# Kernel tuning notes

Measured on AMD Instinct MI355X. Metric: run time of the kernel, lower is better.

## Reference

```python
import jax, jax.numpy as jnp
import numpy as np


def setup_inputs() -> dict:
    key = jax.random.key(0)
    k1, k2, k3, k4 = jax.random.split(key, 4)
    batch, T, state_dim, action_dim = 64, 1024, 512, 128
    x0 = jax.random.normal(k1, (batch, state_dim), dtype=jnp.float32)
    us = jax.random.normal(k2, (batch, T, action_dim), dtype=jnp.float32)
    # Scale A so the 1024-step linear recurrence stays bounded (spectral radius < 1)
    A = jax.random.normal(k3, (state_dim, state_dim), dtype=jnp.float32) * (0.9 / np.sqrt(state_dim))
    B = jax.random.normal(k4, (action_dim, state_dim), dtype=jnp.float32) * (1.0 / np.sqrt(action_dim))
    return {"x0": x0, "us": us, "A": A, "B": B}


def reference(x0, us, A, B):
    """Linear SSM rollout: x_{t+1} = x_t @ A + u_t @ B, returns xs [batch, T, state_dim]."""
    us_t = jnp.swapaxes(us, 0, 1)  # [T, batch, action_dim]

    def step(x, u):
        x_next = x @ A + u @ B  # [batch, state_dim]
        return x_next, x_next

    _, xs = jax.lax.scan(step, x0, us_t)  # xs: [T, batch, state_dim]
    return jnp.swapaxes(xs, 0, 1)  # [batch, T, state_dim]
```

## Files before the change

kernel.cpp:

```cpp
#include <hip/hip_runtime.h>


typedef __attribute__((ext_vector_type(8))) short bf16x8;
typedef __attribute__((ext_vector_type(8))) unsigned short ushort8;
typedef __attribute__((ext_vector_type(4))) float f32x4;
typedef unsigned short ushort_t;

#define MFMA16(a, b, c) __builtin_amdgcn_mfma_f32_16x16x32_bf16(a, b, c, 0, 0, 0)

#define OFF_AT  0UL
#define OFF_AU  8912896UL
#define OFF_BT  15204352UL
#define OFF_BU  15335424UL
#define OFF_WT  15466496UL
#define OFF_Z   16515072UL
#define OFF_E1S 41680896UL
#define OFF_E2S 50069504UL

__host__ __device__ __forceinline__ int slot_of(int p) {
    if (p == 0) return 16;
    if (p <= 8) return p - 1;
    return 7 + (p >> 3);
}

__device__ __forceinline__ unsigned short f2bf(float f) {
    union { float f; unsigned u; } v; v.f = f;
    unsigned r = v.u + 0x7FFFu + ((v.u >> 16) & 1u);
    return (unsigned short)(r >> 16);
}

__device__ __forceinline__ int sel4(int4 v, int p) {
    return p == 0 ? v.x : p == 1 ? v.y : p == 2 ? v.z : v.w;
}

typedef __attribute__((address_space(3))) unsigned int as3_u32;
typedef __attribute__((address_space(1))) const unsigned int as1_u32;
__device__ __forceinline__ void gll16(const void* g, void* l) {
    __builtin_amdgcn_global_load_lds((as1_u32*)g, (as3_u32*)l, 16, 0, 0);
}

__global__ __launch_bounds__(256) void prep_kernel(const float* __restrict__ x0,
                                                   const float* __restrict__ A,
                                                   const float* __restrict__ B,
                                                   char* __restrict__ ws) {
    ushort_t* At1 = (ushort_t*)(ws + OFF_AT);
    ushort_t* Au1 = (ushort_t*)(ws + OFF_AU);
    ushort_t* Bt  = (ushort_t*)(ws + OFF_BT);
    ushort_t* Bu  = (ushort_t*)(ws + OFF_BU);
    ushort_t* X0b = (ushort_t*)(ws + OFF_E2S);
    long idx = (long)blockIdx.x * 256 + threadIdx.x;
    if (idx < 262144) {
        Au1[idx] = f2bf(A[idx]);
    } else if (idx < 524288) {
        long gi = idx - 262144;
        int n = (int)(gi >> 9), k = (int)(gi & 511);
        At1[gi] = f2bf(A[(long)k * 512 + n]);
    } else if (idx < 589824) {
        long i2 = idx - 524288;
        int kp = (int)(i2 >> 9), n = (int)(i2 & 511);
        ushort_t v = f2bf(B[i2]);
        Bt[(long)n * 128 + kp] = v;
        Bu[i2] = v;
    } else if (idx < 593920) {
        long gi = idx - 589824;
        long e0 = gi * 8;
        float4 v0 = *(const float4*)(x0 + e0);
        float4 v1 = *(const float4*)(x0 + e0 + 4);
        ushort8 h = { f2bf(v0.x), f2bf(v0.y), f2bf(v0.z), f2bf(v0.w),
                      f2bf(v1.x), f2bf(v1.y), f2bf(v1.z), f2bf(v1.w) };
        *(ushort8*)(X0b + e0) = h;
    } else {
        long gi2 = idx - 593920;
        if (gi2 < 262144) {
            int n = (int)(gi2 >> 9), k2 = (int)(gi2 & 511);
            At1[(long)16 * 262144 + gi2] = (n == k2) ? (ushort_t)0x3F80 : (ushort_t)0;
        }
    }
}

__device__ __forceinline__ void pow_tile(char* __restrict__ ws, ushort_t* ldsX,
                                         int d, int m_, int i_, int prod,
                                         int mb, int nb) {
    ushort_t* At = (ushort_t*)(ws + OFF_AT);
    ushort_t* Au = (ushort_t*)(ws + OFF_AU);
    const ushort_t *Xp, *Yp; ushort_t* outp;
    if (prod == 0) { Xp = At + (long)slot_of(m_) * 262144; Yp = Au + (long)slot_of(i_) * 262144; outp = At + (long)slot_of(d) * 262144; }
    else           { Xp = Au + (long)slot_of(i_) * 262144; Yp = At + (long)slot_of(m_) * 262144; outp = Au + (long)slot_of(d) * 262144; }

    int tid = threadIdx.x, w = tid >> 6, lane = tid & 63, q = lane >> 4, r = lane & 15;

    for (int i2 = tid; i2 < 64 * 64; i2 += 256) {
        int row = i2 >> 6, c8 = i2 & 63;
        ushort8 v = *(const ushort8*)(Xp + (long)(mb * 64 + row) * 512 + c8 * 8);
        *(ushort8*)&ldsX[row * 512 + ((c8 ^ (row & 7)) << 3)] = v;
    }
    __syncthreads();

    f32x4 acc[4][2];
    for (int a1 = 0; a1 < 4; a1++) for (int b1 = 0; b1 < 2; b1++) acc[a1][b1] = (f32x4){0.f, 0.f, 0.f, 0.f};

    int n0 = nb * 128 + w * 32;
    for (int kt = 0; kt < 16; kt++) {
        bf16x8 b0 = *(const bf16x8*)(Yp + (long)(n0 + r) * 512 + kt * 32 + q * 8);
        bf16x8 b1 = *(const bf16x8*)(Yp + (long)(n0 + 16 + r) * 512 + kt * 32 + q * 8);
        int g2 = kt * 4 + q;
#pragma unroll
        for (int mi = 0; mi < 4; mi++) {
            int row = mi * 16 + r;
            bf16x8 a = *(bf16x8*)&ldsX[row * 512 + ((g2 ^ (row & 7)) << 3)];
            acc[mi][0] = MFMA16(a, b0, acc[mi][0]);
            acc[mi][1] = MFMA16(a, b1, acc[mi][1]);
        }
    }
    for (int mi = 0; mi < 4; mi++) for (int nj = 0; nj < 2; nj++) {
        int m = mb * 64 + mi * 16 + q * 4, n = n0 + nj * 16 + r;
        for (int v = 0; v < 4; v++) outp[(long)(m + v) * 512 + n] = f2bf(acc[mi][nj][v]);
    }
}

__device__ __forceinline__ void wk_tile(char* __restrict__ ws, ushort_t* ldsX,
                                        int k8, int mb) {
    ushort_t* At = (ushort_t*)(ws + OFF_AT);
    ushort_t* Bu = (ushort_t*)(ws + OFF_BU);
    ushort_t* Bt = (ushort_t*)(ws + OFF_BT);
    ushort_t* Wt = (ushort_t*)(ws + OFF_WT);

    int tid = threadIdx.x, w = tid >> 6, lane = tid & 63, q = lane >> 4, r = lane & 15;

    if (k8 == 7) {
        for (int i2 = tid; i2 < 64 * 32; i2 += 256) {
            int row = i2 >> 5, c4 = i2 & 31;
            ushort4 v = *(const ushort4*)(Bt + (long)(mb * 64 + row) * 128 + c4 * 4);
            *(ushort4*)(Wt + (long)(mb * 64 + row) * 128 + c4 * 4) = v;
        }
        return;
    }

    int p = 7 - k8;
    const ushort_t* Xp = At + (long)slot_of(p) * 262144;
    for (int i2 = tid; i2 < 64 * 64; i2 += 256) {
        int row = i2 >> 6, c8 = i2 & 63;
        ushort8 v = *(const ushort8*)(Xp + (long)(mb * 64 + row) * 512 + c8 * 8);
        *(ushort8*)&ldsX[row * 512 + ((c8 ^ (row & 7)) << 3)] = v;
    }
    __syncthreads();

    f32x4 acc[4][2];
    for (int a1 = 0; a1 < 4; a1++) for (int b1 = 0; b1 < 2; b1++) acc[a1][b1] = (f32x4){0.f, 0.f, 0.f, 0.f};

    int n0 = w * 32;
    for (int kt = 0; kt < 16; kt++) {
        bf16x8 b0 = *(const bf16x8*)(Bu + (long)(n0 + r) * 512 + kt * 32 + q * 8);
        bf16x8 b1 = *(const bf16x8*)(Bu + (long)(n0 + 16 + r) * 512 + kt * 32 + q * 8);
        int g2 = kt * 4 + q;
#pragma unroll
        for (int mi = 0; mi < 4; mi++) {
            int row = mi * 16 + r;
            bf16x8 a = *(bf16x8*)&ldsX[row * 512 + ((g2 ^ (row & 7)) << 3)];
            acc[mi][0] = MFMA16(a, b0, acc[mi][0]);
            acc[mi][1] = MFMA16(a, b1, acc[mi][1]);
        }
    }
    ushort_t* Wp = Wt + (long)p * 65536;
    for (int mi = 0; mi < 4; mi++) for (int nj = 0; nj < 2; nj++) {
        int m = mb * 64 + mi * 16 + q * 4, n = n0 + nj * 16 + r;
        for (int v = 0; v < 4; v++) Wp[(long)(m + v) * 128 + n] = f2bf(acc[mi][nj][v]);
    }
}

__global__ __launch_bounds__(256) void pow_stage(char* __restrict__ ws,
                                                 const float* __restrict__ us,
                                                 int4 dd, int4 mm, int4 ii,
                                                 int dual, int wkbase,
                                                 int ubase, int ustart, int uend) {
    __shared__ ushort_t ldsX[64 * 512];
    int bx = blockIdx.x;

    if (ubase > 0 && bx >= ubase) {
        ushort_t* Z = (ushort_t*)(ws + OFF_Z);
        int tid = threadIdx.x;
        int nthr = (256 - ubase) * 256;
        for (long gi = ustart + (long)(bx - ubase) * 256 + tid; gi < uend; gi += nthr) {
            int row = (int)(gi >> 7), g8 = (int)(gi & 127);
            int c = row >> 6, b = row & 63;
            const float* src = us + (long)b * 131072 + c * 1024 + g8 * 8;
            float4 v0 = *(const float4*)src;
            float4 v1 = *(const float4*)(src + 4);
            ushort8 h = { f2bf(v0.x), f2bf(v0.y), f2bf(v0.z), f2bf(v0.w),
                          f2bf(v1.x), f2bf(v1.y), f2bf(v1.z), f2bf(v1.w) };
            *(ushort8*)(Z + (long)row * 1536 + 512 + g8 * 8) = h;
        }
        return;
    }
    if (wkbase > 0 && bx >= wkbase) {
        int widx = bx - wkbase;
        wk_tile(ws, ldsX, widx >> 3, widx & 7);
        return;
    }

    int nb = bx & 3, mb = (bx >> 2) & 7;
    int prod, pair;
    if (dual) { prod = (bx >> 5) & 1; pair = bx >> 6; }
    else      { prod = 0;             pair = bx >> 5; }
    int d = sel4(dd, pair), m_ = sel4(mm, pair), i_ = sel4(ii, pair);
    pow_tile(ws, ldsX, d, m_, i_, prod, mb, nb);
}

__global__ __launch_bounds__(256, 4) void e1g(char* __restrict__ ws) {
    __shared__ ushort_t Alds[64 * 64];
    __shared__ ushort_t Blds[128 * 64];
    const ushort_t* Z  = (const ushort_t*)(ws + OFF_Z);
    const ushort_t* Wt = (const ushort_t*)(ws + OFF_WT);
    ushort_t* E1s = (ushort_t*)(ws + OFF_E1S);

    int bx = blockIdx.x;
    int c = bx >> 2, nt = bx & 3;
    int tid = threadIdx.x, w = tid >> 6, lane = tid & 63, q = lane >> 4, r = lane & 15;
    int wr = w >> 1, wc = w & 1;
    int l8 = lane >> 3, srcg = (lane & 7) ^ l8;

    const ushort_t* Xb = Z + (long)c * 64 * 1536 + 512;

    f32x4 acc[2][4];
#pragma unroll
    for (int a1 = 0; a1 < 2; a1++)
#pragma unroll
        for (int b1 = 0; b1 < 4; b1++) acc[a1][b1] = (f32x4){0.f, 0.f, 0.f, 0.f};

    for (int s = 0; s < 16; s++) {
        int k0 = s * 64;
#pragma unroll
        for (int i = 0; i < 2; i++) {
            int row = i * 32 + w * 8 + l8;
            gll16(Xb + (long)row * 1536 + k0 + srcg * 8, &Alds[i * 2048 + w * 512]);
        }
        const ushort_t* Yb = Wt + (long)(7 - (s >> 1)) * 65536 + (s & 1) * 64;
#pragma unroll
        for (int i = 0; i < 4; i++) {
            int row = i * 32 + w * 8 + l8;
            gll16(Yb + (long)(nt * 128 + row) * 128 + srcg * 8, &Blds[i * 2048 + w * 512]);
        }
        __syncthreads();
#pragma unroll
        for (int kt = 0; kt < 2; kt++) {
            int g2 = kt * 4 + q;
            bf16x8 a[2], b[4];
#pragma unroll
            for (int mi = 0; mi < 2; mi++) {
                int row = wr * 32 + mi * 16 + r;
                a[mi] = *(bf16x8*)&Alds[row * 64 + ((g2 ^ (row & 7)) << 3)];
            }
#pragma unroll
            for (int nj = 0; nj < 4; nj++) {
                int row = wc * 64 + nj * 16 + r;
                b[nj] = *(bf16x8*)&Blds[row * 64 + ((g2 ^ (row & 7)) << 3)];
            }
#pragma unroll
            for (int mi = 0; mi < 2; mi++)
#pragma unroll
                for (int nj = 0; nj < 4; nj++)
                    acc[mi][nj] = MFMA16(a[mi], b[nj], acc[mi][nj]);
        }
        __syncthreads();
    }

#pragma unroll
    for (int mi = 0; mi < 2; mi++)
#pragma unroll
        for (int nj = 0; nj < 4; nj++) {
            int m = wr * 32 + mi * 16 + q * 4;
            int n = nt * 128 + wc * 64 + nj * 16 + r;
#pragma unroll
            for (int v = 0; v < 4; v++)
                E1s[(long)c * 32768 + (long)(m + v) * 512 + n] = f2bf(acc[mi][nj][v]);
        }
}

__global__ __launch_bounds__(256, 4) void e2g(char* __restrict__ ws) {
    __shared__ ushort_t Alds[64 * 64];
    __shared__ ushort_t Blds[32 * 64];
    const ushort_t* At  = (const ushort_t*)(ws + OFF_AT);
    const ushort_t* E1s = (const ushort_t*)(ws + OFF_E1S);
    ushort_t* E2s = (ushort_t*)(ws + OFF_E2S);

    int bx = blockIdx.x;
    int g = bx >> 4, ntb = bx & 15;
    int tid = threadIdx.x, w = tid >> 6, lane = tid & 63, q = lane >> 4, r = lane & 15;
    int wr = w >> 1, wc = w & 1;
    int l8 = lane >> 3, srcg = (lane & 7) ^ l8;

    f32x4 acc[2][1];
#pragma unroll
    for (int a1 = 0; a1 < 2; a1++) acc[a1][0] = (f32x4){0.f, 0.f, 0.f, 0.f};

    for (int s = 0; s < 64; s++) {
        int t = s >> 3, k0 = (s & 7) * 64;
        const ushort_t* Xp = E1s + (long)(8 * g + t) * 32768;
        const ushort_t* Yb = At + (long)slot_of(8 * (7 - t)) * 262144;
#pragma unroll
        for (int i = 0; i < 2; i++) {
            int row = i * 32 + w * 8 + l8;
            gll16(Xp + (long)row * 512 + k0 + srcg * 8, &Alds[i * 2048 + w * 512]);
        }
        {
            int row = w * 8 + l8;
            gll16(Yb + (long)(ntb * 32 + row) * 512 + k0 + srcg * 8, &Blds[w * 512]);
        }
        __syncthreads();
#pragma unroll
        for (int kt = 0; kt < 2; kt++) {
            int g2 = kt * 4 + q;
            bf16x8 a[2], b;
#pragma unroll
            for (int mi = 0; mi < 2; mi++) {
                int row = wr * 32 + mi * 16 + r;
                a[mi] = *(bf16x8*)&Alds[row * 64 + ((g2 ^ (row & 7)) << 3)];
            }
            {
                int row = wc * 16 + r;
                b = *(bf16x8*)&Blds[row * 64 + ((g2 ^ (row & 7)) << 3)];
            }
#pragma unroll
            for (int mi = 0; mi < 2; mi++)
                acc[mi][0] = MFMA16(a[mi], b, acc[mi][0]);
        }
        __syncthreads();
    }

#pragma unroll
    for (int mi = 0; mi < 2; mi++) {
        int m = wr * 32 + mi * 16 + q * 4;
        int n = ntb * 32 + wc * 16 + r;
#pragma unroll
        for (int v = 0; v < 4; v++)
            E2s[(long)(1 + g) * 32768 + (long)(m + v) * 512 + n] = f2bf(acc[mi][0][v]);
    }
}

__global__ __launch_bounds__(256, 4) void s1x(float* __restrict__ dout,
                                              char* __restrict__ ws) {
    __shared__ ushort_t Alds[64 * 64];
    __shared__ ushort_t Blds[128 * 64];
    const ushort_t* At  = (const ushort_t*)(ws + OFF_AT);
    const ushort_t* E1s = (const ushort_t*)(ws + OFF_E1S);
    const ushort_t* E2s = (const ushort_t*)(ws + OFF_E2S);
    ushort_t* Z = (ushort_t*)(ws + OFF_Z);

    int bx = blockIdx.x;
    int t0 = bx >> 2, nt = bx & 3;
    int g, j;
    if (t0 == 128) { g = 16; j = 0; }
    else {
        g = t0 >> 3;
        int jj = t0 & 7;
        j = (g >= 8) ? (7 - jj) : jj;
    }
    int c = g * 8 + j;
    int extra = (j == 0 && g >= 1) ? 1 : 0;
    int nterms = 1 + extra + j;
    int S = nterms * 8;
    int tid = threadIdx.x, w = tid >> 6, lane = tid & 63, q = lane >> 4, r = lane & 15;
    int wr = w >> 1, wc = w & 1;
    int l8 = lane >> 3, srcg = (lane & 7) ^ l8;

    auto xptr = [&](int t) -> const ushort_t* {
        if (t == 0) return E2s + (long)g * 32768;
        if (extra && t == 1) return E2s + (long)(g - 1) * 32768;
        return E1s + (long)(8 * g + t - 1 - extra) * 32768;
    };
    auto yptr = [&](int t) -> const ushort_t* {
        int p = (t == 0) ? 8 * j : ((extra && t == 1) ? 64 : 8 * (j - t + extra));
        return At + (long)slot_of(p) * 262144;
    };

    f32x4 acc[2][4];
#pragma unroll
    for (int a1 = 0; a1 < 2; a1++)
#pragma unroll
        for (int b1 = 0; b1 < 4; b1++) acc[a1][b1] = (f32x4){0.f, 0.f, 0.f, 0.f};

    for (int s = 0; s < S; s++) {
        int t = s >> 3, k0 = (s & 7) * 64;
        const ushort_t* Xp = xptr(t);
        const ushort_t* Yb = yptr(t);
#pragma unroll
        for (int i = 0; i < 2; i++) {
            int row = i * 32 + w * 8 + l8;
            gll16(Xp + (long)row * 512 + k0 + srcg * 8, &Alds[i * 2048 + w * 512]);
        }
#pragma unroll
        for (int i = 0; i < 4; i++) {
            int row = i * 32 + w * 8 + l8;
            gll16(Yb + (long)(nt * 128 + row) * 512 + k0 + srcg * 8, &Blds[i * 2048 + w * 512]);
        }
        __syncthreads();
#pragma unroll
        for (int kt = 0; kt < 2; kt++) {
            int g2 = kt * 4 + q;
            bf16x8 a[2], b[4];
#pragma unroll
            for (int mi = 0; mi < 2; mi++) {
                int row = wr * 32 + mi * 16 + r;
                a[mi] = *(bf16x8*)&Alds[row * 64 + ((g2 ^ (row & 7)) << 3)];
            }
#pragma unroll
            for (int nj = 0; nj < 4; nj++) {
                int row = wc * 64 + nj * 16 + r;
                b[nj] = *(bf16x8*)&Blds[row * 64 + ((g2 ^ (row & 7)) << 3)];
            }
#pragma unroll
            for (int mi = 0; mi < 2; mi++)
#pragma unroll
                for (int nj = 0; nj < 4; nj++)
                    acc[mi][nj] = MFMA16(a[mi], b[nj], acc[mi][nj]);
        }
        __syncthreads();
    }

#pragma unroll
    for (int mi = 0; mi < 2; mi++)
#pragma unroll
        for (int nj = 0; nj < 4; nj++) {
            int m = wr * 32 + mi * 16 + q * 4;
            int n = nt * 128 + wc * 64 + nj * 16 + r;
#pragma unroll
            for (int v = 0; v < 4; v++) {
                float val = acc[mi][nj][v];
                int row = m + v;
                if (c < 128)
                    Z[(long)(c * 64 + row) * 1536 + n] = f2bf(val);
                if (c >= 1)
                    dout[(long)row * 524288 + (long)(8 * c - 1) * 512 + n] = val;
            }
        }
}

__global__ __launch_bounds__(256, 4) void outg(float* __restrict__ dout,
                                               char* __restrict__ ws) {
    __shared__ ushort_t Alds[128 * 64];
    __shared__ ushort_t Blds[128 * 64];
    const ushort_t* Z  = (const ushort_t*)(ws + OFF_Z);
    const ushort_t* At = (const ushort_t*)(ws + OFF_AT);
    const ushort_t* Wt = (const ushort_t*)(ws + OFF_WT);

    int bx = blockIdx.x;
    int nt = bx / 448;
    int rem = bx - nt * 448;
    int k = rem >> 6;
    int mt = rem & 63;
    int tid = threadIdx.x, w = tid >> 6, lane = tid & 63, q = lane >> 4, r = lane & 15;
    int wr = w >> 1, wc = w & 1;
    int l8 = lane >> 3, srcg = (lane & 7) ^ l8;

    const ushort_t* Xb = Z + (long)mt * 128 * 1536;
    const ushort_t* Ya = At + (long)slot_of(k + 1) * 262144;
    int Ks = 8 + 2 * (k + 1);

    f32x4 acc[4][4];
#pragma unroll
    for (int a1 = 0; a1 < 4; a1++)
#pragma unroll
        for (int b1 = 0; b1 < 4; b1++) acc[a1][b1] = (f32x4){0.f, 0.f, 0.f, 0.f};

    for (int s = 0; s < Ks; s++) {
        int k0 = s * 64;
#pragma unroll
        for (int i = 0; i < 4; i++) {
            int row = i * 32 + w * 8 + l8;
            gll16(Xb + (long)row * 1536 + k0 + srcg * 8, &Alds[i * 2048 + w * 512]);
        }
        if (k0 < 512) {
#pragma unroll
            for (int i = 0; i < 4; i++) {
                int row = i * 32 + w * 8 + l8;
                gll16(Ya + (long)(nt * 128 + row) * 512 + k0 + srcg * 8, &Blds[i * 2048 + w * 512]);
            }
        } else {
            int uc = k0 - 512;
            const ushort_t* Yb = Wt + (long)(k - (uc >> 7)) * 65536 + (uc & 127);
#pragma unroll
            for (int i = 0; i < 4; i++) {
                int row = i * 32 + w * 8 + l8;
                gll16(Yb + (long)(nt * 128 + row) * 128 + srcg * 8, &Blds[i * 2048 + w * 512]);
            }
        }
        __syncthreads();
#pragma unroll
        for (int kt = 0; kt < 2; kt++) {
            int g2 = kt * 4 + q;
            bf16x8 a[4], b[4];
#pragma unroll
            for (int mi = 0; mi < 4; mi++) {
                int row = wr * 64 + mi * 16 + r;
                a[mi] = *(bf16x8*)&Alds[row * 64 + ((g2 ^ (row & 7)) << 3)];
            }
#pragma unroll
            for (int nj = 0; nj < 4; nj++) {
                int row = wc * 64 + nj * 16 + r;
                b[nj] = *(bf16x8*)&Blds[row * 64 + ((g2 ^ (row & 7)) << 3)];
            }
#pragma unroll
            for (int mi = 0; mi < 4; mi++)
#pragma unroll
                for (int nj = 0; nj < 4; nj++)
                    acc[mi][nj] = MFMA16(a[mi], b[nj], acc[mi][nj]);
        }
        __syncthreads();
    }

#pragma unroll
    for (int mi = 0; mi < 4; mi++) {
        int m = mt * 128 + wr * 64 + mi * 16 + q * 4;
#pragma unroll
        for (int nj = 0; nj < 4; nj++) {
            int n = nt * 128 + wc * 64 + nj * 16 + r;
#pragma unroll
            for (int v = 0; v < 4; v++) {
                int mm = m + v;
                dout[(long)(mm & 63) * 524288 + (long)(((mm >> 6) << 3) + k) * 512 + n] = acc[mi][nj][v];
            }
        }
    }
}

extern "C" void kernel_launch(void* const* d_in, const int* in_sizes, int n_in,
                              void* d_out, int out_size, void* d_ws, size_t ws_size,
                              hipStream_t stream) {
    const float* x0 = (const float*)d_in[0];
    const float* us = (const float*)d_in[1];
    const float* A  = (const float*)d_in[2];
    const float* B  = (const float*)d_in[3];
    float* dout = (float*)d_out;
    char* ws = (char*)d_ws;

    prep_kernel<<<3344, 256, 0, stream>>>(x0, A, B, ws);

    const int stpw[6]    = {64, 128, 256, 64, 128, 128};
    const int stdual[6]  = {1, 1, 1, 1, 1, 0};
    const int stwk[6]    = {0, 0, 0, 64, 0, 0};
    const int stub[6]    = {64, 128, 0, 128, 128, 128};
    const int stus[6]    = {0, 262144, 0, 458752, 655360, 851968};
    const int stue[6]    = {262144, 458752, 0, 655360, 851968, 1048576};
    const int std_[6][4] = {{2,0,0,0},{3,4,0,0},{5,6,7,8},{16,0,0,0},{24,32,0,0},{40,48,56,64}};
    const int stm[6][4]  = {{1,0,0,0},{2,2,0,0},{4,4,4,4},{8,0,0,0},{16,16,0,0},{32,32,32,32}};
    const int sti[6][4]  = {{1,0,0,0},{1,2,0,0},{1,2,3,4},{8,0,0,0},{8,16,0,0},{8,16,24,32}};
    for (int s = 0; s < 6; s++) {
        int4 dd = {std_[s][0], std_[s][1], std_[s][2], std_[s][3]};
        int4 mm = {stm[s][0], stm[s][1], stm[s][2], stm[s][3]};
        int4 ii = {sti[s][0], sti[s][1], sti[s][2], sti[s][3]};
        int blocks = (stub[s] > 0) ? 256 : stpw[s] + stwk[s];
        pow_stage<<<blocks, 256, 0, stream>>>(ws, us, dd, mm, ii, stdual[s],
                                              stwk[s], stub[s], stus[s], stue[s]);
    }

    e1g<<<512, 256, 0, stream>>>(ws);
    e2g<<<256, 256, 0, stream>>>(ws);
    s1x<<<516, 256, 0, stream>>>(dout, ws);
    outg<<<1792, 256, 0, stream>>>(dout, ws);
}
```

Measured before the change: 253.0 us.

## Fold B/x0/identity prep into pow stages, split e2g M, raise occupancy

Moves the B transpose, x0 conversion and identity-matrix fill out of the prep kernel into otherwise idle blocks of the first power stage, and rebalances the us conversion ranges across later stages. e2g is split along M into two half-tiles, doubling its grid for more parallelism. Launch bounds on the GEMM kernels are raised from 4 to 5 waves per SIMD to allow more resident blocks, which may increase register pressure or spills.

```diff
diff --git a/kernel.cpp b/kernel.cpp
--- a/kernel.cpp
+++ b/kernel.cpp
@@ -39,42 +39,17 @@
     __builtin_amdgcn_global_load_lds((as1_u32*)g, (as3_u32*)l, 16, 0, 0);
 }
 
-__global__ __launch_bounds__(256) void prep_kernel(const float* __restrict__ x0,
-                                                   const float* __restrict__ A,
-                                                   const float* __restrict__ B,
+__global__ __launch_bounds__(256) void prep_kernel(const float* __restrict__ A,
                                                    char* __restrict__ ws) {
     ushort_t* At1 = (ushort_t*)(ws + OFF_AT);
     ushort_t* Au1 = (ushort_t*)(ws + OFF_AU);
-    ushort_t* Bt  = (ushort_t*)(ws + OFF_BT);
-    ushort_t* Bu  = (ushort_t*)(ws + OFF_BU);
-    ushort_t* X0b = (ushort_t*)(ws + OFF_E2S);
     long idx = (long)blockIdx.x * 256 + threadIdx.x;
     if (idx < 262144) {
         Au1[idx] = f2bf(A[idx]);
-    } else if (idx < 524288) {
+    } else {
         long gi = idx - 262144;
         int n = (int)(gi >> 9), k = (int)(gi & 511);
         At1[gi] = f2bf(A[(long)k * 512 + n]);
-    } else if (idx < 589824) {
-        long i2 = idx - 524288;
-        int kp = (int)(i2 >> 9), n = (int)(i2 & 511);
-        ushort_t v = f2bf(B[i2]);
-        Bt[(long)n * 128 + kp] = v;
-        Bu[i2] = v;
-    } else if (idx < 593920) {
-        long gi = idx - 589824;
-        long e0 = gi * 8;
-        float4 v0 = *(const float4*)(x0 + e0);
-        float4 v1 = *(const float4*)(x0 + e0 + 4);
-        ushort8 h = { f2bf(v0.x), f2bf(v0.y), f2bf(v0.z), f2bf(v0.w),
-                      f2bf(v1.x), f2bf(v1.y), f2bf(v1.z), f2bf(v1.w) };
-        *(ushort8*)(X0b + e0) = h;
-    } else {
-        long gi2 = idx - 593920;
-        if (gi2 < 262144) {
-            int n = (int)(gi2 >> 9), k2 = (int)(gi2 & 511);
-            At1[(long)16 * 262144 + gi2] = (n == k2) ? (ushort_t)0x3F80 : (ushort_t)0;
-        }
     }
 }
 
@@ -170,25 +145,55 @@
 
 __global__ __launch_bounds__(256) void pow_stage(char* __restrict__ ws,
                                                  const float* __restrict__ us,
+                                                 const float* __restrict__ x0,
+                                                 const float* __restrict__ B,
                                                  int4 dd, int4 mm, int4 ii,
                                                  int dual, int wkbase,
-                                                 int ubase, int ustart, int uend) {
+                                                 int ubase, int umode,
+                                                 int ustart, int uend) {
     __shared__ ushort_t ldsX[64 * 512];
     int bx = blockIdx.x;
 
     if (ubase > 0 && bx >= ubase) {
-        ushort_t* Z = (ushort_t*)(ws + OFF_Z);
         int tid = threadIdx.x;
         int nthr = (256 - ubase) * 256;
-        for (long gi = ustart + (long)(bx - ubase) * 256 + tid; gi < uend; gi += nthr) {
-            int row = (int)(gi >> 7), g8 = (int)(gi & 127);
-            int c = row >> 6, b = row & 63;
-            const float* src = us + (long)b * 131072 + c * 1024 + g8 * 8;
-            float4 v0 = *(const float4*)src;
-            float4 v1 = *(const float4*)(src + 4);
-            ushort8 h = { f2bf(v0.x), f2bf(v0.y), f2bf(v0.z), f2bf(v0.w),
-                          f2bf(v1.x), f2bf(v1.y), f2bf(v1.z), f2bf(v1.w) };
-            *(ushort8*)(Z + (long)row * 1536 + 512 + g8 * 8) = h;
+        if (umode == 0) {
+            ushort_t* Z = (ushort_t*)(ws + OFF_Z);
+            for (long gi = ustart + (long)(bx - ubase) * 256 + tid; gi < uend; gi += nthr) {
+                int row = (int)(gi >> 7), g8 = (int)(gi & 127);
+                int c = row >> 6, b = row & 63;
+                const float* src = us + (long)b * 131072 + c * 1024 + g8 * 8;
+                float4 v0 = *(const float4*)src;
+                float4 v1 = *(const float4*)(src + 4);
+                ushort8 h = { f2bf(v0.x), f2bf(v0.y), f2bf(v0.z), f2bf(v0.w),
+                              f2bf(v1.x), f2bf(v1.y), f2bf(v1.z), f2bf(v1.w) };
+                *(ushort8*)(Z + (long)row * 1536 + 512 + g8 * 8) = h;
+            }
+        } else {
+            ushort_t* Bt  = (ushort_t*)(ws + OFF_BT);
+            ushort_t* Bu  = (ushort_t*)(ws + OFF_BU);
+            ushort_t* X0b = (ushort_t*)(ws + OFF_E2S);
+            ushort_t* At1 = (ushort_t*)(ws + OFF_AT);
+            for (long i = (long)(bx - ubase) * 256 + tid; i < 331776; i += nthr) {
+                if (i < 65536) {
+                    int kp = (int)(i >> 9), n = (int)(i & 511);
+                    ushort_t v = f2bf(B[i]);
+                    Bt[(long)n * 128 + kp] = v;
+                    Bu[i] = v;
+                } else if (i < 69632) {
+                    long gi = i - 65536;
+                    long e0 = gi * 8;
+                    float4 v0 = *(const float4*)(x0 + e0);
+                    float4 v1 = *(const float4*)(x0 + e0 + 4);
+                    ushort8 h = { f2bf(v0.x), f2bf(v0.y), f2bf(v0.z), f2bf(v0.w),
+                                  f2bf(v1.x), f2bf(v1.y), f2bf(v1.z), f2bf(v1.w) };
+                    *(ushort8*)(X0b + e0) = h;
+                } else {
+                    long gi2 = i - 69632;
+                    int n = (int)(gi2 >> 9), k2 = (int)(gi2 & 511);
+                    At1[(long)16 * 262144 + gi2] = (n == k2) ? (ushort_t)0x3F80 : (ushort_t)0;
+                }
+            }
         }
         return;
     }
@@ -206,7 +211,7 @@
     pow_tile(ws, ldsX, d, m_, i_, prod, mb, nb);
 }
 
-__global__ __launch_bounds__(256, 4) void e1g(char* __restrict__ ws) {
+__global__ __launch_bounds__(256, 5) void e1g(char* __restrict__ ws) {
     __shared__ ushort_t Alds[64 * 64];
     __shared__ ushort_t Blds[128 * 64];
     const ushort_t* Z  = (const ushort_t*)(ws + OFF_Z);
@@ -276,68 +281,53 @@
         }
 }
 
-__global__ __launch_bounds__(256, 4) void e2g(char* __restrict__ ws) {
-    __shared__ ushort_t Alds[64 * 64];
+__global__ __launch_bounds__(256, 5) void e2g(char* __restrict__ ws) {
+    __shared__ ushort_t Alds[32 * 64];
     __shared__ ushort_t Blds[32 * 64];
     const ushort_t* At  = (const ushort_t*)(ws + OFF_AT);
     const ushort_t* E1s = (const ushort_t*)(ws + OFF_E1S);
     ushort_t* E2s = (ushort_t*)(ws + OFF_E2S);
 
     int bx = blockIdx.x;
-    int g = bx >> 4, ntb = bx & 15;
+    int g = bx >> 5, mb = (bx >> 4) & 1, ntb = bx & 15;
     int tid = threadIdx.x, w = tid >> 6, lane = tid & 63, q = lane >> 4, r = lane & 15;
     int wr = w >> 1, wc = w & 1;
     int l8 = lane >> 3, srcg = (lane & 7) ^ l8;
 
-    f32x4 acc[2][1];
-#pragma unroll
-    for (int a1 = 0; a1 < 2; a1++) acc[a1][0] = (f32x4){0.f, 0.f, 0.f, 0.f};
+    f32x4 acc = (f32x4){0.f, 0.f, 0.f, 0.f};
 
     for (int s = 0; s < 64; s++) {
         int t = s >> 3, k0 = (s & 7) * 64;
-        const ushort_t* Xp = E1s + (long)(8 * g + t) * 32768;
+        const ushort_t* Xp = E1s + (long)(8 * g + t) * 32768 + (long)mb * 32 * 512;
         const ushort_t* Yb = At + (long)slot_of(8 * (7 - t)) * 262144;
-#pragma unroll
-        for (int i = 0; i < 2; i++) {
-            int row = i * 32 + w * 8 + l8;
-            gll16(Xp + (long)row * 512 + k0 + srcg * 8, &Alds[i * 2048 + w * 512]);
-        }
         {
             int row = w * 8 + l8;
+            gll16(Xp + (long)row * 512 + k0 + srcg * 8, &Alds[w * 512]);
             gll16(Yb + (long)(ntb * 32 + row) * 512 + k0 + srcg * 8, &Blds[w * 512]);
         }
         __syncthreads();
 #pragma unroll
         for (int kt = 0; kt < 2; kt++) {
             int g2 = kt * 4 + q;
-            bf16x8 a[2], b;
-#pragma unroll
-            for (int mi = 0; mi < 2; mi++) {
-                int row = wr * 32 + mi * 16 + r;
-                a[mi] = *(bf16x8*)&Alds[row * 64 + ((g2 ^ (row & 7)) << 3)];
-            }
-            {
-                int row = wc * 16 + r;
-                b = *(bf16x8*)&Blds[row * 64 + ((g2 ^ (row & 7)) << 3)];
-            }
-#pragma unroll
-            for (int mi = 0; mi < 2; mi++)
-                acc[mi][0] = MFMA16(a[mi], b, acc[mi][0]);
-        }
-        __syncthreads();
-    }
-
-#pragma unroll
-    for (int mi = 0; mi < 2; mi++) {
-        int m = wr * 32 + mi * 16 + q * 4;
+            int arow = wr * 16 + r;
+            bf16x8 a = *(bf16x8*)&Alds[arow * 64 + ((g2 ^ (arow & 7)) << 3)];
+            int brow = wc * 16 + r;
+            bf16x8 b = *(bf16x8*)&Blds[brow * 64 + ((g2 ^ (brow & 7)) << 3)];
+            acc = MFMA16(a, b, acc);
+        }
+        __syncthreads();
+    }
+
+    {
+        int m = mb * 32 + wr * 16 + q * 4;
         int n = ntb * 32 + wc * 16 + r;
 #pragma unroll
         for (int v = 0; v < 4; v++)
-            E2s[(long)(1 + g) * 32768 + (long)(m + v) * 512 + n] = f2bf(acc[mi][0][v]);
-    }
-}
-
-__global__ __launch_bounds__(256, 4) void s1x(float* __restrict__ dout,
+            E2s[(long)(1 + g) * 32768 + (long)(m + v) * 512 + n] = f2bf(acc[v]);
+    }
+}
+
+__global__ __launch_bounds__(256, 5) void s1x(float* __restrict__ dout,
                                               char* __restrict__ ws) {
     __shared__ ushort_t Alds[64 * 64];
     __shared__ ushort_t Blds[128 * 64];
@@ -435,7 +425,7 @@
         }
 }
 
-__global__ __launch_bounds__(256, 4) void outg(float* __restrict__ dout,
+__global__ __launch_bounds__(256, 5) void outg(float* __restrict__ dout,
                                                char* __restrict__ ws) {
     __shared__ ushort_t Alds[128 * 64];
     __shared__ ushort_t Blds[128 * 64];
@@ -533,14 +523,15 @@
     float* dout = (float*)d_out;
     char* ws = (char*)d_ws;
 
-    prep_kernel<<<3344, 256, 0, stream>>>(x0, A, B, ws);
-
-    const int stpw[6]    = {64, 128, 256, 64, 128, 128};
+    prep_kernel<<<2048, 256, 0, stream>>>(A, ws);
+
     const int stdual[6]  = {1, 1, 1, 1, 1, 0};
     const int stwk[6]    = {0, 0, 0, 64, 0, 0};
     const int stub[6]    = {64, 128, 0, 128, 128, 128};
-    const int stus[6]    = {0, 262144, 0, 458752, 655360, 851968};
-    const int stue[6]    = {262144, 458752, 0, 655360, 851968, 1048576};
+    const int stum[6]    = {1, 0, 0, 0, 0, 0};
+    const int stus[6]    = {0, 0, 0, 262144, 524288, 786432};
+    const int stue[6]    = {0, 262144, 0, 524288, 786432, 1048576};
+    const int stpw[6]    = {64, 128, 256, 64, 128, 128};
     const int std_[6][4] = {{2,0,0,0},{3,4,0,0},{5,6,7,8},{16,0,0,0},{24,32,0,0},{40,48,56,64}};
     const int stm[6][4]  = {{1,0,0,0},{2,2,0,0},{4,4,4,4},{8,0,0,0},{16,16,0,0},{32,32,32,32}};
     const int sti[6][4]  = {{1,0,0,0},{1,2,0,0},{1,2,3,4},{8,0,0,0},{8,16,0,0},{8,16,24,32}};
@@ -549,12 +540,13 @@
         int4 mm = {stm[s][0], stm[s][1], stm[s][2], stm[s][3]};
         int4 ii = {sti[s][0], sti[s][1], sti[s][2], sti[s][3]};
         int blocks = (stub[s] > 0) ? 256 : stpw[s] + stwk[s];
-        pow_stage<<<blocks, 256, 0, stream>>>(ws, us, dd, mm, ii, stdual[s],
-                                              stwk[s], stub[s], stus[s], stue[s]);
+        pow_stage<<<blocks, 256, 0, stream>>>(ws, us, x0, B, dd, mm, ii,
+                                              stdual[s], stwk[s], stub[s],
+                                              stum[s], stus[s], stue[s]);
     }
 
     e1g<<<512, 256, 0, stream>>>(ws);
-    e2g<<<256, 256, 0, stream>>>(ws);
+    e2g<<<512, 256, 0, stream>>>(ws);
     s1x<<<516, 256, 0, stream>>>(dout, ws);
     outg<<<1792, 256, 0, stream>>>(dout, ws);
 }
```

New measurement: 283.3 us. +12.0%, slower.
